# Optimization experiments

Hardware: AMD Instinct MI355X
Metric: run time of the kernel (lower is better)

## Reference

```python
import jax, jax.numpy as jnp
import numpy as np

# 27 kernel taps x 3 offset components (dz, dy, dx), matching the module's offset0 list.
OFFSET0 = np.array([
    1, 1, 1, 1, 1, 0, 1, 1, -1, 1, 0, 1, 1, 0, 0, 1, 0, -1, 1, -1, 1, 1, -1, 0, 1, -1, -1,
    0, 1, 1, 0, 1, 0, 0, 1, -1, 0, 0, 1, 0, 0, 0, 0, 0, -1, 0, -1, 1, 0, -1, 0, 0, -1, -1,
    -1, 1, 1, -1, 1, 0, -1, 1, -1, -1, 0, 1, -1, 0, 0, -1, 0, -1, -1, -1, 1, -1, -1, 0, -1, -1, -1
], dtype=np.float64).reshape(27, 3)

BN_EPS = 1e-5


def upsample_nearest2(x):
    # nn.Upsample(scale_factor=2), default mode='nearest', on [B,C,Z,Y,X]
    x = jnp.repeat(x, 2, axis=2)
    x = jnp.repeat(x, 2, axis=3)
    return jnp.repeat(x, 2, axis=4)


def deform_conv3d_static(x, W, b, alpha):
    """3D deformable conv, kernel 3, pad 1, stride 1, with spatially-constant
    per-tap offsets alpha*OFFSET0. Zero padding outside; trilinear sampling.
    Since offsets are static, each tap samples at a fixed fractional shift,
    implemented as a static trilinear combination of slices of the padded input.
    x: [B,C,Z,Y,X], W: [O,C,3,3,3], b: [O].
    """
    B, C, Z, Y, X = x.shape
    # pad 2: 1 for the 3x3x3 kernel + 1 for fractional offsets (|alpha*d| <= 0.7)
    xp = jnp.pad(x, ((0, 0), (0, 0), (2, 2), (2, 2), (2, 2)))
    out = None
    t = 0
    for kz in range(3):
        for ky in range(3):
            for kx in range(3):
                dz, dy, dx = (alpha * OFFSET0[t]).tolist()
                s = (kz - 1 + dz, ky - 1 + dy, kx - 1 + dx)  # shift rel. to output voxel
                f = [int(np.floor(v)) for v in s]
                w = [v - fl for v, fl in zip(s, f)]
                vol = None
                for cz in (0, 1):
                    for cy in (0, 1):
                        for cx in (0, 1):
                            wt = ((w[0] if cz else 1.0 - w[0]) *
                                  (w[1] if cy else 1.0 - w[1]) *
                                  (w[2] if cx else 1.0 - w[2]))
                            if wt == 0.0:
                                continue
                            z0 = 2 + f[0] + cz
                            y0 = 2 + f[1] + cy
                            x0 = 2 + f[2] + cx
                            sl = xp[:, :, z0:z0 + Z, y0:y0 + Y, x0:x0 + X]
                            sl = jnp.float32(wt) * sl
                            vol = sl if vol is None else vol + sl
                contrib = jnp.einsum('oc,bczyx->bozyx', W[:, :, kz, ky, kx], vol)
                out = contrib if out is None else out + contrib
                t += 1
    return out + b[None, :, None, None, None]


def batchnorm(x, g, bt, m, v):
    # eval-mode BatchNorm3d over channel axis 1
    inv = g * jax.lax.rsqrt(v + BN_EPS)
    return x * inv[None, :, None, None, None] + (bt - m * inv)[None, :, None, None, None]


def setup_inputs() -> dict:
    key = jax.random.key(0)
    ks = jax.random.split(key, 13)
    ch_in, ch_out = 64, 32
    x = jax.random.normal(ks[0], (1, ch_in, 32, 32, 32), jnp.float32)
    w_def = jax.random.normal(ks[1], (ch_out, ch_in, 3, 3, 3), jnp.float32) * 0.05
    b_def = jax.random.normal(ks[2], (ch_out,), jnp.float32) * 0.05
    bn1_g = 1.0 + 0.1 * jax.random.normal(ks[3], (ch_out,), jnp.float32)
    bn1_b = 0.1 * jax.random.normal(ks[4], (ch_out,), jnp.float32)
    bn1_m = 0.1 * jax.random.normal(ks[5], (ch_out,), jnp.float32)
    bn1_v = jax.random.uniform(ks[6], (ch_out,), jnp.float32, 0.5, 1.5)
    w_comb = jax.random.normal(ks[7], (ch_out, 3 * ch_out), jnp.float32) * 0.1
    b_comb = 0.05 * jax.random.normal(ks[8], (ch_out,), jnp.float32)
    bn2_g = 1.0 + 0.1 * jax.random.normal(ks[9], (ch_out,), jnp.float32)
    bn2_b = 0.1 * jax.random.normal(ks[10], (ch_out,), jnp.float32)
    bn2_m = 0.1 * jax.random.normal(ks[11], (ch_out,), jnp.float32)
    bn2_v = jax.random.uniform(ks[12], (ch_out,), jnp.float32, 0.5, 1.5)
    return {"x": x, "w_def": w_def, "b_def": b_def,
            "bn1_g": bn1_g, "bn1_b": bn1_b, "bn1_m": bn1_m, "bn1_v": bn1_v,
            "w_comb": w_comb, "b_comb": b_comb,
            "bn2_g": bn2_g, "bn2_b": bn2_b, "bn2_m": bn2_m, "bn2_v": bn2_v}


def reference(x, w_def, b_def, bn1_g, bn1_b, bn1_m, bn1_v,
              w_comb, b_comb, bn2_g, bn2_b, bn2_m, bn2_v):
    xu = upsample_nearest2(x)
    branches = []
    for alpha in (0.0, 0.4, 0.7):  # shared deform-conv weights, three static offset scales
        o = deform_conv3d_static(xu, w_def, b_def, alpha)
        o = jax.nn.relu(batchnorm(o, bn1_g, bn1_b, bn1_m, bn1_v))
        branches.append(o)
    cat = jnp.concatenate(branches, axis=1)  # [B, 3*ch_out, Z,Y,X]
    y = jnp.einsum('oc,bczyx->bozyx', w_comb, cat) + b_comb[None, :, None, None, None]
    y = batchnorm(y, bn2_g, bn2_b, bn2_m, bn2_v)
    return jax.nn.relu(y)
```

## Files before the change

### kernel.cpp

```cpp
#include <hip/hip_runtime.h>


typedef __bf16 bf16x8 __attribute__((ext_vector_type(8)));
typedef float f32x4 __attribute__((ext_vector_type(4)));

__device__ inline unsigned short f2bf(float f) {
  unsigned int u = __float_as_uint(f);
  u += 0x7FFFu + ((u >> 16) & 1u);
  return (unsigned short)(u >> 16);
}

__device__ inline bf16x8 bc16(uint4 v) { return __builtin_bit_cast(bf16x8, v); }

__device__ inline unsigned cvtpk(float lo, float hi) {
  unsigned r;
  asm("v_cvt_pk_bf16_f32 %0, %1, %2" : "=v"(r) : "v"(lo), "v"(hi));
  return r;
}

__device__ inline void gload16(const unsigned short* g, unsigned short* l) {
  __builtin_amdgcn_global_load_lds(
      (const __attribute__((address_space(1))) unsigned int*)(const void*)g,
      (__attribute__((address_space(3))) unsigned int*)(void*)l, 16, 0, 0);
}

__device__ inline float ucoef(int abit, int k, int jbit, float alpha) {
  if (abit == 0) return (k == 0) ? (jbit ? alpha : 1.f - alpha) : (jbit ? 1.f : 0.f);
  return (k == 2) ? (jbit ? 1.f - alpha : alpha) : (jbit ? 0.f : 1.f);
}

#define XREG_USH 524352
#define XZERO_B 1048576u

__global__ void k_prep(const float* __restrict__ x, unsigned short* __restrict__ xT2,
                       const float* __restrict__ w_def, const float* __restrict__ bn1_g,
                       const float* __restrict__ bn1_v, unsigned short* __restrict__ W_sw,
                       const float* __restrict__ w_comb, const float* __restrict__ b_comb,
                       const float* __restrict__ bn2_g, const float* __restrict__ bn2_b,
                       const float* __restrict__ bn2_m, const float* __restrict__ bn2_v,
                       const float* __restrict__ b_def, const float* __restrict__ bn1_b,
                       const float* __restrict__ bn1_m, unsigned short* __restrict__ W2_sw,
                       float* __restrict__ bias1, float* __restrict__ bias2) {
  __shared__ unsigned short t[64][65];
  int bid = blockIdx.x;
  if (bid < 512) {
    int s0 = bid * 64;
    int lane = threadIdx.x & 63;
    int grp = threadIdx.x >> 6;
#pragma unroll
    for (int c = grp; c < 64; c += 4)
      t[c][lane] = f2bf(x[c * 32768 + s0 + lane]);
    __syncthreads();
    int q = lane >> 4, e = lane & 15;
#pragma unroll
    for (int s = grp; s < 64; s += 4)
      xT2[q * XREG_USH + (size_t)(s0 + s) * 16 + e] = t[lane][s];
  } else if (bid < 2048) {
    int e = (bid - 512) * 256 + threadIdx.x;
    int j = e & 7;
    int lane = (e >> 3) & 63;
    int idx = e >> 9;
    int ntile = idx % 6;
    int idx2 = idx / 6;
    int kstep = idx2 & 15;
    int p = idx2 >> 4;
    int n = ntile * 16 + (lane & 15);
    int o = n & 31, br = n >> 5;
    int k = (kstep << 5) + ((lane >> 4) << 3) + j;
    int tap = k >> 6, ch = k & 63;
    int jz = (tap >> 2) & 1, jy = (tap >> 1) & 1, jx = tap & 1;
    int a = (p >> 2) & 1, b = (p >> 1) & 1, cp = p & 1;
    float alpha = (br == 0) ? 0.f : ((br == 1) ? 0.4f : 0.7f);
    const float* wb = w_def + (o * 64 + ch) * 27;
    float sum = 0.f;
    for (int kz = 0; kz < 3; ++kz) {
      float uz = ucoef(a, kz, jz, alpha);
      if (uz == 0.f) continue;
      for (int ky = 0; ky < 3; ++ky) {
        float uy = ucoef(b, ky, jy, alpha);
        if (uy == 0.f) continue;
        float uzy = uz * uy;
        for (int kx = 0; kx < 3; ++kx) {
          float ux = ucoef(cp, kx, jx, alpha);
          if (ux != 0.f) sum += wb[kz * 9 + ky * 3 + kx] * uzy * ux;
        }
      }
    }
    float s1 = bn1_g[o] * rsqrtf(bn1_v[o] + 1e-5f);
    W_sw[e] = f2bf(sum * s1);
  } else {
    int tid = threadIdx.x;
    for (int e = tid; e < 3072; e += 256) {
      int j = e & 7;
      int lane = (e >> 3) & 63;
      int idx = e >> 9;
      int ks2 = idx % 3, n2t = idx / 3;
      int n2 = n2t * 16 + (lane & 15);
      int k2 = (ks2 << 5) + ((lane >> 4) << 3) + j;
      int pch = (2 * (k2 >> 5) + ((k2 & 7) >> 2)) * 16 + 4 * ((k2 & 31) >> 3) + (k2 & 3);
      float sc2 = bn2_g[n2] * rsqrtf(bn2_v[n2] + 1e-5f);
      W2_sw[e] = f2bf(w_comb[n2 * 96 + pch] * sc2);
    }
    {
      int q = tid >> 6, e2 = tid & 63;
      xT2[q * XREG_USH + 524288 + e2] = 0;
    }
    if (tid < 32) {
      float s1 = bn1_g[tid] * rsqrtf(bn1_v[tid] + 1e-5f);
      bias1[tid] = (b_def[tid] - bn1_m[tid]) * s1 + bn1_b[tid];
      float s2 = bn2_g[tid] * rsqrtf(bn2_v[tid] + 1e-5f);
      bias2[tid] = (b_comb[tid] - bn2_m[tid]) * s2 + bn2_b[tid];
    }
  }
}

__launch_bounds__(256, 3)
__global__ void k_main(const unsigned short* __restrict__ xT2,
                       const unsigned short* __restrict__ W_sw,
                       const unsigned short* __restrict__ W2_sw,
                       const float* __restrict__ bias1f,
                       const float* __restrict__ bias2f,
                       float* __restrict__ out) {
  __shared__ unsigned short wring[2][12288];
  __shared__ float blds[128];
  int tid = threadIdx.x;
  int lane = tid & 63;
  int wv = tid >> 6;
  int bid = blockIdx.x;
  int tb = (bid & 7) | ((bid >> 5) << 3);
  int ph = (bid >> 3) & 3;
  int bph = ph & 1, a = ph >> 1;
  int tx = tb & 3, ty = (tb >> 2) & 7, tz = tb >> 5;
  int i0 = tz * 4, j0 = ty * 4, k0 = tx * 8;

  if (tid < 96) blds[tid] = bias1f[tid & 31];
  else if (tid < 128) blds[tid] = bias2f[tid - 96];

  int m = lane & 15, hi = lane >> 4;
  int ax = m & 7, ay = m >> 3;
  int p0 = (a << 2) | (bph << 1);
  const char* xb0 = (const char*)xT2 + (size_t)(hi >> 1) * 1048704 + ((hi & 1) << 4);

  auto stage = [&](int cc) {
    int pn = p0 | (cc >> 2);
    const unsigned short* g =
        W_sw + pn * 49152 + (cc & 3) * 12288 + wv * 3072 + lane * 8;
    unsigned short* l = &wring[cc & 1][wv * 3072];
#pragma unroll
    for (int k = 0; k < 6; ++k) gload16(g + k * 512, l + k * 512);
  };

  __syncthreads();
  stage(0);

  const f32x4* b1v = (const f32x4*)blds;
  const f32x4* b2v = (const f32x4*)(blds + 96);
  const uint4* w2q = (const uint4*)W2_sw;

  f32x4 osv[2][2];
  f32x4 acc[2][6];
#pragma unroll
  for (int mt = 0; mt < 2; ++mt)
#pragma unroll
    for (int nt = 0; nt < 6; ++nt) acc[mt][nt] = (f32x4)0.f;

  for (int cc = 0; cc < 8; ++cc) {
    asm volatile("s_waitcnt vmcnt(0)" ::: "memory");
    __builtin_amdgcn_s_barrier();
    __builtin_amdgcn_sched_barrier(0);
    if (cc < 7) stage(cc + 1);
    __builtin_amdgcn_sched_barrier(0);

    int cp = cc >> 2;
    unsigned xoff[2][2];
#pragma unroll
    for (int tl = 0; tl < 2; ++tl) {
      int tap = 2 * (cc & 3) + tl;
      int jz = (tap >> 2) & 1, jy = (tap >> 1) & 1, jx = tap & 1;
      int gz = i0 + wv + a - 1 + jz;
      int gx = k0 + ax + cp - 1 + jx;
#pragma unroll
      for (int mt = 0; mt < 2; ++mt) {
        int gy = j0 + 2 * mt + ay + bph - 1 + jy;
        bool ok = ((unsigned)gz < 32u) && ((unsigned)gy < 32u) && ((unsigned)gx < 32u);
        unsigned off = (unsigned)(((gz * 32 + gy) * 32 + gx) * 32);
        xoff[tl][mt] = ok ? off : XZERO_B;
      }
    }

    const unsigned short* wcb = &wring[cc & 1][lane * 8];
#pragma unroll
    for (int ksl = 0; ksl < 4; ++ksl) {
      int tl = ksl >> 1, khalf = ksl & 1;
      const char* xp = xb0 + khalf * 2097408;
      bf16x8 x0 = bc16(*(const uint4*)(xp + xoff[tl][0]));
      bf16x8 x1 = bc16(*(const uint4*)(xp + xoff[tl][1]));
      const unsigned short* wk = wcb + ksl * 3072;
      bf16x8 w0 = bc16(*(const uint4*)(wk));
      bf16x8 w1 = bc16(*(const uint4*)(wk + 512));
      bf16x8 w2 = bc16(*(const uint4*)(wk + 1024));
      bf16x8 w3 = bc16(*(const uint4*)(wk + 1536));
      bf16x8 w4 = bc16(*(const uint4*)(wk + 2048));
      bf16x8 w5 = bc16(*(const uint4*)(wk + 2560));
      __builtin_amdgcn_s_setprio(1);
      acc[0][0] = __builtin_amdgcn_mfma_f32_16x16x32_bf16(w0, x0, acc[0][0], 0, 0, 0);
      acc[1][0] = __builtin_amdgcn_mfma_f32_16x16x32_bf16(w0, x1, acc[1][0], 0, 0, 0);
      acc[0][1] = __builtin_amdgcn_mfma_f32_16x16x32_bf16(w1, x0, acc[0][1], 0, 0, 0);
      acc[1][1] = __builtin_amdgcn_mfma_f32_16x16x32_bf16(w1, x1, acc[1][1], 0, 0, 0);
      acc[0][2] = __builtin_amdgcn_mfma_f32_16x16x32_bf16(w2, x0, acc[0][2], 0, 0, 0);
      acc[1][2] = __builtin_amdgcn_mfma_f32_16x16x32_bf16(w2, x1, acc[1][2], 0, 0, 0);
      acc[0][3] = __builtin_amdgcn_mfma_f32_16x16x32_bf16(w3, x0, acc[0][3], 0, 0, 0);
      acc[1][3] = __builtin_amdgcn_mfma_f32_16x16x32_bf16(w3, x1, acc[1][3], 0, 0, 0);
      acc[0][4] = __builtin_amdgcn_mfma_f32_16x16x32_bf16(w4, x0, acc[0][4], 0, 0, 0);
      acc[1][4] = __builtin_amdgcn_mfma_f32_16x16x32_bf16(w4, x1, acc[1][4], 0, 0, 0);
      acc[0][5] = __builtin_amdgcn_mfma_f32_16x16x32_bf16(w5, x0, acc[0][5], 0, 0, 0);
      acc[1][5] = __builtin_amdgcn_mfma_f32_16x16x32_bf16(w5, x1, acc[1][5], 0, 0, 0);
      __builtin_amdgcn_s_setprio(0);
    }

    if (cc == 3) {
#pragma unroll
      for (int mt = 0; mt < 2; ++mt) {
        uint4 fr[3];
#pragma unroll
        for (int ks2 = 0; ks2 < 3; ++ks2) {
          f32x4 vA = acc[mt][2 * ks2], vB = acc[mt][2 * ks2 + 1];
          f32x4 bA = b1v[(2 * ks2) * 4 + hi], bB = b1v[(2 * ks2 + 1) * 4 + hi];
          fr[ks2] = make_uint4(
              cvtpk(fmaxf(vA[0] + bA[0], 0.f), fmaxf(vA[1] + bA[1], 0.f)),
              cvtpk(fmaxf(vA[2] + bA[2], 0.f), fmaxf(vA[3] + bA[3], 0.f)),
              cvtpk(fmaxf(vB[0] + bB[0], 0.f), fmaxf(vB[1] + bB[1], 0.f)),
              cvtpk(fmaxf(vB[2] + bB[2], 0.f), fmaxf(vB[3] + bB[3], 0.f)));
        }
        f32x4 a20 = (f32x4)0.f, a21 = (f32x4)0.f;
#pragma unroll
        for (int ks2 = 0; ks2 < 3; ++ks2) {
          a20 = __builtin_amdgcn_mfma_f32_16x16x32_bf16(bc16(w2q[ks2 * 64 + lane]),
                                                        bc16(fr[ks2]), a20, 0, 0, 0);
          a21 = __builtin_amdgcn_mfma_f32_16x16x32_bf16(bc16(w2q[(3 + ks2) * 64 + lane]),
                                                        bc16(fr[ks2]), a21, 0, 0, 0);
        }
        f32x4 b20 = b2v[hi], b21 = b2v[4 + hi];
#pragma unroll
        for (int r = 0; r < 4; ++r) {
          osv[mt][0][r] = fmaxf(a20[r] + b20[r], 0.f);
          osv[mt][1][r] = fmaxf(a21[r] + b21[r], 0.f);
        }
#pragma unroll
        for (int nt = 0; nt < 6; ++nt) acc[mt][nt] = (f32x4)0.f;
      }
    }
  }

#pragma unroll
  for (int mt = 0; mt < 2; ++mt) {
    uint4 fr[3];
#pragma unroll
    for (int ks2 = 0; ks2 < 3; ++ks2) {
      f32x4 vA = acc[mt][2 * ks2], vB = acc[mt][2 * ks2 + 1];
      f32x4 bA = b1v[(2 * ks2) * 4 + hi], bB = b1v[(2 * ks2 + 1) * 4 + hi];
      fr[ks2] = make_uint4(
          cvtpk(fmaxf(vA[0] + bA[0], 0.f), fmaxf(vA[1] + bA[1], 0.f)),
          cvtpk(fmaxf(vA[2] + bA[2], 0.f), fmaxf(vA[3] + bA[3], 0.f)),
          cvtpk(fmaxf(vB[0] + bB[0], 0.f), fmaxf(vB[1] + bB[1], 0.f)),
          cvtpk(fmaxf(vB[2] + bB[2], 0.f), fmaxf(vB[3] + bB[3], 0.f)));
    }
    f32x4 a20 = (f32x4)0.f, a21 = (f32x4)0.f;
#pragma unroll
    for (int ks2 = 0; ks2 < 3; ++ks2) {
      a20 = __builtin_amdgcn_mfma_f32_16x16x32_bf16(bc16(w2q[ks2 * 64 + lane]),
                                                    bc16(fr[ks2]), a20, 0, 0, 0);
      a21 = __builtin_amdgcn_mfma_f32_16x16x32_bf16(bc16(w2q[(3 + ks2) * 64 + lane]),
                                                    bc16(fr[ks2]), a21, 0, 0, 0);
    }
    f32x4 b20 = b2v[hi], b21 = b2v[4 + hi];
    int Z = 2 * (i0 + wv) + a;
    int Y = 2 * (j0 + 2 * mt + ay) + bph;
    size_t sb = ((size_t)Z << 11) + (Y << 5) + (k0 + ax);
    float2* o2 = (float2*)out;
#pragma unroll
    for (int r = 0; r < 4; ++r) {
      int ch0 = 4 * hi + r, ch1 = 16 + 4 * hi + r;
      o2[((size_t)ch0 << 17) + sb] =
          make_float2(osv[mt][0][r], fmaxf(a20[r] + b20[r], 0.f));
      o2[((size_t)ch1 << 17) + sb] =
          make_float2(osv[mt][1][r], fmaxf(a21[r] + b21[r], 0.f));
    }
  }
}

extern "C" void kernel_launch(void* const* d_in, const int* in_sizes, int n_in,
                              void* d_out, int out_size, void* d_ws, size_t ws_size,
                              hipStream_t stream) {
  (void)in_sizes; (void)n_in; (void)out_size; (void)ws_size;
  const float* x      = (const float*)d_in[0];
  const float* w_def  = (const float*)d_in[1];
  const float* b_def  = (const float*)d_in[2];
  const float* bn1_g  = (const float*)d_in[3];
  const float* bn1_b  = (const float*)d_in[4];
  const float* bn1_m  = (const float*)d_in[5];
  const float* bn1_v  = (const float*)d_in[6];
  const float* w_comb = (const float*)d_in[7];
  const float* b_comb = (const float*)d_in[8];
  const float* bn2_g  = (const float*)d_in[9];
  const float* bn2_b  = (const float*)d_in[10];
  const float* bn2_m  = (const float*)d_in[11];
  const float* bn2_v  = (const float*)d_in[12];

  char* ws = (char*)d_ws;
  unsigned short* xT2  = (unsigned short*)(ws);
  unsigned short* W_sw = (unsigned short*)(ws + 4194816);
  unsigned short* W2sw = (unsigned short*)(ws + 4981248);
  float* bias1 = (float*)(ws + 4987392);
  float* bias2 = (float*)(ws + 4987520);
  float* out = (float*)d_out;

  hipLaunchKernelGGL(k_prep, dim3(2049), dim3(256), 0, stream,
                     x, xT2, w_def, bn1_g, bn1_v, W_sw,
                     w_comb, b_comb, bn2_g, bn2_b, bn2_m, bn2_v,
                     b_def, bn1_b, bn1_m, W2sw, bias1, bias2);
  hipLaunchKernelGGL(k_main, dim3(1024), dim3(256), 0, stream,
                     xT2, W_sw, W2sw, bias1, bias2, out);
}
```

Baseline: 54.12 us.

## Read conv weights directly from global and shrink blocks to two waves

Removes the double-buffered LDS weight ring, its async global-to-LDS staging and the per-step barriers. Each wave now loads its MFMA weight fragments straight from global memory through the caches, in a fully unrolled loop over the two x-phases. Bias vectors move from LDS into registers. Blocks shrink to 128 threads with twice as many blocks, halving the z-extent per block. The aim is to cut synchronisation and LDS traffic, at the cost of redundant per-wave weight fetches through L1/L2 and more register pressure from full unrolling.

New measurement: 100.2 us. 85.1% more time.

```diff
diff --git a/kernel.cpp b/kernel.cpp
--- a/kernel.cpp
+++ b/kernel.cpp
@@ -16,12 +16,6 @@
   unsigned r;
   asm("v_cvt_pk_bf16_f32 %0, %1, %2" : "=v"(r) : "v"(lo), "v"(hi));
   return r;
-}
-
-__device__ inline void gload16(const unsigned short* g, unsigned short* l) {
-  __builtin_amdgcn_global_load_lds(
-      (const __attribute__((address_space(1))) unsigned int*)(const void*)g,
-      (__attribute__((address_space(3))) unsigned int*)(void*)l, 16, 0, 0);
 }
 
 __device__ inline float ucoef(int abit, int k, int jbit, float alpha) {
@@ -114,15 +108,13 @@
   }
 }
 
-__launch_bounds__(256, 3)
+__launch_bounds__(128, 3)
 __global__ void k_main(const unsigned short* __restrict__ xT2,
                        const unsigned short* __restrict__ W_sw,
                        const unsigned short* __restrict__ W2_sw,
                        const float* __restrict__ bias1f,
                        const float* __restrict__ bias2f,
                        float* __restrict__ out) {
-  __shared__ unsigned short wring[2][12288];
-  __shared__ float blds[128];
   int tid = threadIdx.x;
   int lane = tid & 63;
   int wv = tid >> 6;
@@ -131,78 +123,60 @@
   int ph = (bid >> 3) & 3;
   int bph = ph & 1, a = ph >> 1;
   int tx = tb & 3, ty = (tb >> 2) & 7, tz = tb >> 5;
-  int i0 = tz * 4, j0 = ty * 4, k0 = tx * 8;
-
-  if (tid < 96) blds[tid] = bias1f[tid & 31];
-  else if (tid < 128) blds[tid] = bias2f[tid - 96];
+  int i0 = tz * 2, j0 = ty * 4, k0 = tx * 8;
 
   int m = lane & 15, hi = lane >> 4;
   int ax = m & 7, ay = m >> 3;
   int p0 = (a << 2) | (bph << 1);
   const char* xb0 = (const char*)xT2 + (size_t)(hi >> 1) * 1048704 + ((hi & 1) << 4);
 
-  auto stage = [&](int cc) {
-    int pn = p0 | (cc >> 2);
-    const unsigned short* g =
-        W_sw + pn * 49152 + (cc & 3) * 12288 + wv * 3072 + lane * 8;
-    unsigned short* l = &wring[cc & 1][wv * 3072];
-#pragma unroll
-    for (int k = 0; k < 6; ++k) gload16(g + k * 512, l + k * 512);
-  };
-
-  __syncthreads();
-  stage(0);
-
-  const f32x4* b1v = (const f32x4*)blds;
-  const f32x4* b2v = (const f32x4*)(blds + 96);
+  f32x4 b1v[6], b2v[2];
+#pragma unroll
+  for (int nt = 0; nt < 6; ++nt)
+#pragma unroll
+    for (int r = 0; r < 4; ++r) b1v[nt][r] = bias1f[(nt * 16 + 4 * hi + r) & 31];
+#pragma unroll
+  for (int r = 0; r < 4; ++r) {
+    b2v[0][r] = bias2f[4 * hi + r];
+    b2v[1][r] = bias2f[16 + 4 * hi + r];
+  }
+
   const uint4* w2q = (const uint4*)W2_sw;
-
   f32x4 osv[2][2];
-  f32x4 acc[2][6];
-#pragma unroll
-  for (int mt = 0; mt < 2; ++mt)
-#pragma unroll
-    for (int nt = 0; nt < 6; ++nt) acc[mt][nt] = (f32x4)0.f;
-
-  for (int cc = 0; cc < 8; ++cc) {
-    asm volatile("s_waitcnt vmcnt(0)" ::: "memory");
-    __builtin_amdgcn_s_barrier();
-    __builtin_amdgcn_sched_barrier(0);
-    if (cc < 7) stage(cc + 1);
-    __builtin_amdgcn_sched_barrier(0);
-
-    int cp = cc >> 2;
-    unsigned xoff[2][2];
-#pragma unroll
-    for (int tl = 0; tl < 2; ++tl) {
-      int tap = 2 * (cc & 3) + tl;
+
+#pragma unroll
+  for (int cp = 0; cp < 2; ++cp) {
+    const uint4* wp = (const uint4*)(W_sw + (size_t)(p0 | cp) * 49152) + lane;
+    f32x4 acc[2][6];
+#pragma unroll
+    for (int mt = 0; mt < 2; ++mt)
+#pragma unroll
+      for (int nt = 0; nt < 6; ++nt) acc[mt][nt] = (f32x4)0.f;
+
+#pragma unroll
+    for (int ks = 0; ks < 16; ++ks) {
+      int tap = ks >> 1, khalf = ks & 1;
       int jz = (tap >> 2) & 1, jy = (tap >> 1) & 1, jx = tap & 1;
       int gz = i0 + wv + a - 1 + jz;
       int gx = k0 + ax + cp - 1 + jx;
+      const char* xp = xb0 + khalf * 2097408;
+      unsigned xo[2];
 #pragma unroll
       for (int mt = 0; mt < 2; ++mt) {
         int gy = j0 + 2 * mt + ay + bph - 1 + jy;
         bool ok = ((unsigned)gz < 32u) && ((unsigned)gy < 32u) && ((unsigned)gx < 32u);
         unsigned off = (unsigned)(((gz * 32 + gy) * 32 + gx) * 32);
-        xoff[tl][mt] = ok ? off : XZERO_B;
-      }
-    }
-
-    const unsigned short* wcb = &wring[cc & 1][lane * 8];
-#pragma unroll
-    for (int ksl = 0; ksl < 4; ++ksl) {
-      int tl = ksl >> 1, khalf = ksl & 1;
-      const char* xp = xb0 + khalf * 2097408;
-      bf16x8 x0 = bc16(*(const uint4*)(xp + xoff[tl][0]));
-      bf16x8 x1 = bc16(*(const uint4*)(xp + xoff[tl][1]));
-      const unsigned short* wk = wcb + ksl * 3072;
-      bf16x8 w0 = bc16(*(const uint4*)(wk));
-      bf16x8 w1 = bc16(*(const uint4*)(wk + 512));
-      bf16x8 w2 = bc16(*(const uint4*)(wk + 1024));
-      bf16x8 w3 = bc16(*(const uint4*)(wk + 1536));
-      bf16x8 w4 = bc16(*(const uint4*)(wk + 2048));
-      bf16x8 w5 = bc16(*(const uint4*)(wk + 2560));
-      __builtin_amdgcn_s_setprio(1);
+        xo[mt] = ok ? off : XZERO_B;
+      }
+      bf16x8 x0 = bc16(*(const uint4*)(xp + xo[0]));
+      bf16x8 x1 = bc16(*(const uint4*)(xp + xo[1]));
+      const uint4* wk = wp + ks * 384;
+      bf16x8 w0 = bc16(wk[0]);
+      bf16x8 w1 = bc16(wk[64]);
+      bf16x8 w2 = bc16(wk[128]);
+      bf16x8 w3 = bc16(wk[192]);
+      bf16x8 w4 = bc16(wk[256]);
+      bf16x8 w5 = bc16(wk[320]);
       acc[0][0] = __builtin_amdgcn_mfma_f32_16x16x32_bf16(w0, x0, acc[0][0], 0, 0, 0);
       acc[1][0] = __builtin_amdgcn_mfma_f32_16x16x32_bf16(w0, x1, acc[1][0], 0, 0, 0);
       acc[0][1] = __builtin_amdgcn_mfma_f32_16x16x32_bf16(w1, x0, acc[0][1], 0, 0, 0);
@@ -215,17 +189,16 @@
       acc[1][4] = __builtin_amdgcn_mfma_f32_16x16x32_bf16(w4, x1, acc[1][4], 0, 0, 0);
       acc[0][5] = __builtin_amdgcn_mfma_f32_16x16x32_bf16(w5, x0, acc[0][5], 0, 0, 0);
       acc[1][5] = __builtin_amdgcn_mfma_f32_16x16x32_bf16(w5, x1, acc[1][5], 0, 0, 0);
-      __builtin_amdgcn_s_setprio(0);
-    }
-
-    if (cc == 3) {
+    }
+
+    if (cp == 0) {
 #pragma unroll
       for (int mt = 0; mt < 2; ++mt) {
         uint4 fr[3];
 #pragma unroll
         for (int ks2 = 0; ks2 < 3; ++ks2) {
           f32x4 vA = acc[mt][2 * ks2], vB = acc[mt][2 * ks2 + 1];
-          f32x4 bA = b1v[(2 * ks2) * 4 + hi], bB = b1v[(2 * ks2 + 1) * 4 + hi];
+          f32x4 bA = b1v[2 * ks2], bB = b1v[2 * ks2 + 1];
           fr[ks2] = make_uint4(
               cvtpk(fmaxf(vA[0] + bA[0], 0.f), fmaxf(vA[1] + bA[1], 0.f)),
               cvtpk(fmaxf(vA[2] + bA[2], 0.f), fmaxf(vA[3] + bA[3], 0.f)),
@@ -240,51 +213,47 @@
           a21 = __builtin_amdgcn_mfma_f32_16x16x32_bf16(bc16(w2q[(3 + ks2) * 64 + lane]),
                                                         bc16(fr[ks2]), a21, 0, 0, 0);
         }
-        f32x4 b20 = b2v[hi], b21 = b2v[4 + hi];
 #pragma unroll
         for (int r = 0; r < 4; ++r) {
-          osv[mt][0][r] = fmaxf(a20[r] + b20[r], 0.f);
-          osv[mt][1][r] = fmaxf(a21[r] + b21[r], 0.f);
-        }
-#pragma unroll
-        for (int nt = 0; nt < 6; ++nt) acc[mt][nt] = (f32x4)0.f;
-      }
-    }
-  }
-
-#pragma unroll
-  for (int mt = 0; mt < 2; ++mt) {
-    uint4 fr[3];
-#pragma unroll
-    for (int ks2 = 0; ks2 < 3; ++ks2) {
-      f32x4 vA = acc[mt][2 * ks2], vB = acc[mt][2 * ks2 + 1];
-      f32x4 bA = b1v[(2 * ks2) * 4 + hi], bB = b1v[(2 * ks2 + 1) * 4 + hi];
-      fr[ks2] = make_uint4(
-          cvtpk(fmaxf(vA[0] + bA[0], 0.f), fmaxf(vA[1] + bA[1], 0.f)),
-          cvtpk(fmaxf(vA[2] + bA[2], 0.f), fmaxf(vA[3] + bA[3], 0.f)),
-          cvtpk(fmaxf(vB[0] + bB[0], 0.f), fmaxf(vB[1] + bB[1], 0.f)),
-          cvtpk(fmaxf(vB[2] + bB[2], 0.f), fmaxf(vB[3] + bB[3], 0.f)));
-    }
-    f32x4 a20 = (f32x4)0.f, a21 = (f32x4)0.f;
-#pragma unroll
-    for (int ks2 = 0; ks2 < 3; ++ks2) {
-      a20 = __builtin_amdgcn_mfma_f32_16x16x32_bf16(bc16(w2q[ks2 * 64 + lane]),
-                                                    bc16(fr[ks2]), a20, 0, 0, 0);
-      a21 = __builtin_amdgcn_mfma_f32_16x16x32_bf16(bc16(w2q[(3 + ks2) * 64 + lane]),
-                                                    bc16(fr[ks2]), a21, 0, 0, 0);
-    }
-    f32x4 b20 = b2v[hi], b21 = b2v[4 + hi];
-    int Z = 2 * (i0 + wv) + a;
-    int Y = 2 * (j0 + 2 * mt + ay) + bph;
-    size_t sb = ((size_t)Z << 11) + (Y << 5) + (k0 + ax);
-    float2* o2 = (float2*)out;
-#pragma unroll
-    for (int r = 0; r < 4; ++r) {
-      int ch0 = 4 * hi + r, ch1 = 16 + 4 * hi + r;
-      o2[((size_t)ch0 << 17) + sb] =
-          make_float2(osv[mt][0][r], fmaxf(a20[r] + b20[r], 0.f));
-      o2[((size_t)ch1 << 17) + sb] =
-          make_float2(osv[mt][1][r], fmaxf(a21[r] + b21[r], 0.f));
+          osv[mt][0][r] = fmaxf(a20[r] + b2v[0][r], 0.f);
+          osv[mt][1][r] = fmaxf(a21[r] + b2v[1][r], 0.f);
+        }
+      }
+    } else {
+#pragma unroll
+      for (int mt = 0; mt < 2; ++mt) {
+        uint4 fr[3];
+#pragma unroll
+        for (int ks2 = 0; ks2 < 3; ++ks2) {
+          f32x4 vA = acc[mt][2 * ks2], vB = acc[mt][2 * ks2 + 1];
+          f32x4 bA = b1v[2 * ks2], bB = b1v[2 * ks2 + 1];
+          fr[ks2] = make_uint4(
+              cvtpk(fmaxf(vA[0] + bA[0], 0.f), fmaxf(vA[1] + bA[1], 0.f)),
+              cvtpk(fmaxf(vA[2] + bA[2], 0.f), fmaxf(vA[3] + bA[3], 0.f)),
+              cvtpk(fmaxf(vB[0] + bB[0], 0.f), fmaxf(vB[1] + bB[1], 0.f)),
+              cvtpk(fmaxf(vB[2] + bB[2], 0.f), fmaxf(vB[3] + bB[3], 0.f)));
+        }
+        f32x4 a20 = (f32x4)0.f, a21 = (f32x4)0.f;
+#pragma unroll
+        for (int ks2 = 0; ks2 < 3; ++ks2) {
+          a20 = __builtin_amdgcn_mfma_f32_16x16x32_bf16(bc16(w2q[ks2 * 64 + lane]),
+                                                        bc16(fr[ks2]), a20, 0, 0, 0);
+          a21 = __builtin_amdgcn_mfma_f32_16x16x32_bf16(bc16(w2q[(3 + ks2) * 64 + lane]),
+                                                        bc16(fr[ks2]), a21, 0, 0, 0);
+        }
+        int Z = 2 * (i0 + wv) + a;
+        int Y = 2 * (j0 + 2 * mt + ay) + bph;
+        size_t sb = ((size_t)Z << 11) + (Y << 5) + (k0 + ax);
+        float2* o2 = (float2*)out;
+#pragma unroll
+        for (int r = 0; r < 4; ++r) {
+          int ch0 = 4 * hi + r, ch1 = 16 + 4 * hi + r;
+          o2[((size_t)ch0 << 17) + sb] =
+              make_float2(osv[mt][0][r], fmaxf(a20[r] + b2v[0][r], 0.f));
+          o2[((size_t)ch1 << 17) + sb] =
+              make_float2(osv[mt][1][r], fmaxf(a21[r] + b2v[1][r], 0.f));
+        }
+      }
     }
   }
 }
@@ -319,6 +288,6 @@
                      x, xT2, w_def, bn1_g, bn1_v, W_sw,
                      w_comb, b_comb, bn2_g, bn2_b, bn2_m, bn2_v,
                      b_def, bn1_b, bn1_m, W2sw, bias1, bias2);
-  hipLaunchKernelGGL(k_main, dim3(1024), dim3(256), 0, stream,
+  hipLaunchKernelGGL(k_main, dim3(2048), dim3(128), 0, stream,
                      xT2, W_sw, W2sw, bias1, bias2, out);
 }
```
